# Optimization experiments

Measured on AMD Instinct MI355X. Metric: run time of the kernel, lower is better.

## Reference

```python
import jax, jax.numpy as jnp
import numpy as np

# 8 neighbor offsets (dy, dx) in unfold row-major order with center (0,0) removed
NEIGHBOR_OFFSETS = [(-1, -1), (-1, 0), (-1, 1), (0, -1), (0, 1), (1, -1), (1, 0), (1, 1)]


def setup_inputs() -> dict:
    key = jax.random.key(0)
    B, H, W, L, C = 8, 16, 16, 64, 64
    E_flat = jax.random.normal(key, (B, H * W, L, C), dtype=jnp.float32)
    return {"E_flat": E_flat, "H": H, "W": W}


def reference(E_flat, H, W):
    B, P, L, C = E_flat.shape
    assert P == H * W
    # restore grid: [B, H, W, L, C]
    E_grid = E_flat.reshape(B, H, W, L, C)
    # zero-pad spatial dims by 1 (matches nn.Unfold padding=1)
    pad = jnp.pad(E_grid, ((0, 0), (1, 1), (1, 1), (0, 0), (0, 0)))
    # gather 8 shifted views; stack on new axis after L -> [B, H, W, L, 8, C]
    neigh = jnp.stack(
        [pad[:, 1 + dy:1 + dy + H, 1 + dx:1 + dx + W] for dy, dx in NEIGHBOR_OFFSETS],
        axis=4,
    )
    # [B, patches, length*8, input_size]
    return neigh.reshape(B, H * W, L * 8, C)
```

## Files before the change

### kernel.cpp

```cpp
#include <hip/hip_runtime.h>


typedef float f32x4 __attribute__((ext_vector_type(4)));

constexpr unsigned IN4 = 8u * 256u * 64u * 16u;

__global__ __launch_bounds__(256) void patch_scatter(
    const f32x4* __restrict__ in, f32x4* __restrict__ out) {
  const unsigned i = blockIdx.x * 256u + threadIdx.x;
  const unsigned c4 = i & 15u;
  const unsigned l  = (i >> 4) & 63u;
  const unsigned p  = (i >> 10) & 255u;
  const unsigned b  = i >> 18;
  const int h = (int)(p >> 4);
  const int w = (int)(p & 15u);

  const f32x4 v = __builtin_nontemporal_load(&in[i]);
  const f32x4 z = {0.f, 0.f, 0.f, 0.f};

  const unsigned obase = (b << 21) | (l << 7) | c4;
  const unsigned zbase = obase | (p << 13);

  constexpr int DY[8] = {-1, -1, -1,  0, 0,  1, 1, 1};
  constexpr int DX[8] = {-1,  0,  1, -1, 1, -1, 0, 1};
#pragma unroll
  for (int n = 0; n < 8; ++n) {
    const int hh = h - DY[n];
    const int ww = w - DX[n];
    if (((unsigned)hh < 16u) & ((unsigned)ww < 16u)) {
      const unsigned dst =
          obase | ((unsigned)((hh << 4) | ww) << 13) | ((unsigned)n << 4);
      __builtin_nontemporal_store(v, &out[dst]);
    }
    const int h2 = h + DY[n];
    const int w2 = w + DX[n];
    if (!(((unsigned)h2 < 16u) & ((unsigned)w2 < 16u))) {
      __builtin_nontemporal_store(z, &out[zbase | ((unsigned)n << 4)]);
    }
  }
}

extern "C" void kernel_launch(void* const* d_in, const int* in_sizes, int n_in,
                              void* d_out, int out_size, void* d_ws, size_t ws_size,
                              hipStream_t stream) {
  const f32x4* in = (const f32x4*)d_in[0];
  f32x4* out = (f32x4*)d_out;
  patch_scatter<<<IN4 / 256u, 256, 0, stream>>>(in, out);
}
```

Before: 283.5 us.

## Replace scatter with coalesced gather using per-thread ILP and block swizzle

Rewrites the kernel from a per-input scatter into a per-output gather. Each thread loads 8 neighbor vectors, clamping addresses and zeroing the out-of-bounds ones, then writes fully contiguous output rows. Block IDs are swizzled across 8 groups, and the nontemporal hints are dropped. The aim is to turn the scattered writes into contiguous ones and raise memory-level parallelism. The cost is that each input is now read up to 8 times, relying on caches to absorb the extra reads.

```diff
diff --git a/kernel.cpp b/kernel.cpp
--- a/kernel.cpp
+++ b/kernel.cpp
@@ -3,40 +3,47 @@
 
 typedef float f32x4 __attribute__((ext_vector_type(4)));
 
-constexpr unsigned IN4 = 8u * 256u * 64u * 16u;
-
-__global__ __launch_bounds__(256) void patch_scatter(
+__global__ __launch_bounds__(256) void patch_gather_ilp(
     const f32x4* __restrict__ in, f32x4* __restrict__ out) {
-  const unsigned i = blockIdx.x * 256u + threadIdx.x;
-  const unsigned c4 = i & 15u;
-  const unsigned l  = (i >> 4) & 63u;
-  const unsigned p  = (i >> 10) & 255u;
-  const unsigned b  = i >> 18;
-  const int h = (int)(p >> 4);
-  const int w = (int)(p & 15u);
-
-  const f32x4 v = __builtin_nontemporal_load(&in[i]);
-  const f32x4 z = {0.f, 0.f, 0.f, 0.f};
-
-  const unsigned obase = (b << 21) | (l << 7) | c4;
-  const unsigned zbase = obase | (p << 13);
+  unsigned id = (blockIdx.x & 7u) * 1024u + (blockIdx.x >> 3);
+  const unsigned lq = id & 3u;
+  const unsigned p  = (id >> 2) & 255u;
+  const unsigned b  = id >> 10;
+  const unsigned wv = threadIdx.x >> 6;
+  const unsigned ln = threadIdx.x & 63u;
+  const unsigned c4 = ln & 15u;
+  const unsigned g  = ln >> 4;
+  const int h = (int)(p >> 4), w = (int)(p & 15u);
+  const unsigned l0 = lq * 16u + wv * 4u;
 
   constexpr int DY[8] = {-1, -1, -1,  0, 0,  1, 1, 1};
   constexpr int DX[8] = {-1,  0,  1, -1, 1, -1, 0, 1};
+
+  const f32x4 z = {0.f, 0.f, 0.f, 0.f};
+  f32x4 v[8];
+
 #pragma unroll
-  for (int n = 0; n < 8; ++n) {
-    const int hh = h - DY[n];
-    const int ww = w - DX[n];
-    if (((unsigned)hh < 16u) & ((unsigned)ww < 16u)) {
-      const unsigned dst =
-          obase | ((unsigned)((hh << 4) | ww) << 13) | ((unsigned)n << 4);
-      __builtin_nontemporal_store(v, &out[dst]);
-    }
-    const int h2 = h + DY[n];
-    const int w2 = w + DX[n];
-    if (!(((unsigned)h2 < 16u) & ((unsigned)w2 < 16u))) {
-      __builtin_nontemporal_store(z, &out[zbase | ((unsigned)n << 4)]);
-    }
+  for (int j = 0; j < 8; ++j) {
+    const unsigned n  = (unsigned)((j & 1) * 4) + g;
+    const unsigned lp = l0 + (unsigned)(j >> 1);
+    const int hh = h + DY[n];
+    const int ww = w + DX[n];
+    const bool ok = ((unsigned)hh < 16u) & ((unsigned)ww < 16u);
+    const int hc = min(max(hh, 0), 15);
+    const int wc = min(max(ww, 0), 15);
+    const unsigned src = (b << 18) | ((unsigned)((hc << 4) | wc) << 10) |
+                         (lp << 4) | c4;
+    const f32x4 t = in[src];
+    v[j].x = ok ? t.x : z.x;
+    v[j].y = ok ? t.y : z.y;
+    v[j].z = ok ? t.z : z.z;
+    v[j].w = ok ? t.w : z.w;
+  }
+
+  const unsigned ob = (b << 21) | (p << 13) | (l0 << 7);
+#pragma unroll
+  for (int j = 0; j < 8; ++j) {
+    out[ob + (unsigned)j * 64u + ln] = v[j];
   }
 }
 
@@ -45,5 +52,5 @@
                               hipStream_t stream) {
   const f32x4* in = (const f32x4*)d_in[0];
   f32x4* out = (f32x4*)d_out;
-  patch_scatter<<<IN4 / 256u, 256, 0, stream>>>(in, out);
+  patch_gather_ilp<<<8192, 256, 0, stream>>>(in, out);
 }
```

Result: slower. 306.1 us (+8.0%).
